# Kernel optimization log

Hardware: AMD Instinct MI355X
Metric: run time of the kernel (lower is better)

Reference implementation:

```python
import jax, jax.numpy as jnp
import numpy as np

N, E = 100000, 250000
SD, CD = 128, 768


def setup_inputs() -> dict:
    key = jax.random.key(0)
    ks = jax.random.split(key, 12)
    z = jax.random.normal(ks[0], (N, SD), dtype=jnp.float32)
    chemistry = jax.random.normal(ks[1], (N, CD), dtype=jnp.float32)
    edge = jax.random.randint(ks[2], (E, 2), 0, N, dtype=jnp.int64)
    smiles_mask = (jax.random.uniform(ks[3], (N,)) < 0.8).astype(jnp.float32)
    s = 1.0 / np.sqrt(SD)
    W1s = jax.random.uniform(ks[4], (SD, SD // 2), jnp.float32, -s, s)
    b1s = jax.random.uniform(ks[5], (SD // 2,), jnp.float32, -s, s)
    s2 = 1.0 / np.sqrt(SD // 2)
    W2s = jax.random.uniform(ks[6], (SD // 2, 1), jnp.float32, -s2, s2)
    b2s = jax.random.uniform(ks[7], (1,), jnp.float32, -s2, s2)
    c = 1.0 / np.sqrt(CD)
    W1c = jax.random.uniform(ks[8], (CD, CD // 4), jnp.float32, -c, c)
    b1c = jax.random.uniform(ks[9], (CD // 4,), jnp.float32, -c, c)
    c2 = 1.0 / np.sqrt(CD // 4)
    W2c = jax.random.uniform(ks[10], (CD // 4, 1), jnp.float32, -c2, c2)
    b2c = jax.random.uniform(ks[11], (1,), jnp.float32, -c2, c2)
    alpha = jnp.float32(0.1)
    return {"z": z, "chemistry": chemistry, "edge": edge, "smiles_mask": smiles_mask,
            "W1s": W1s, "b1s": b1s, "W2s": W2s, "b2s": b2s,
            "W1c": W1c, "b1c": b1c, "W2c": W2c, "b2c": b2c, "alpha": alpha}


def reference(z, chemistry, edge, smiles_mask, W1s, b1s, W2s, b2s,
              W1c, b1c, W2c, b2c, alpha):
    src, dst = edge[:, 0], edge[:, 1]
    # structural branch: gather, product, 2-layer MLP (dropout = eval identity)
    structural_prod = z[src] * z[dst]                      # [E, SD]
    h_s = jax.nn.relu(structural_prod @ W1s + b1s)         # [E, SD//2]
    score_structural = (h_s @ W2s + b2s)[:, 0]             # [E]
    # chemical branch
    chemical_prod = chemistry[src] * chemistry[dst]        # [E, CD]
    h_c = jax.nn.relu(chemical_prod @ W1c + b1c)           # [E, CD//4]
    score_chemical = (h_c @ W2c + b2c)[:, 0]               # [E]
    both_valid = smiles_mask[src] * smiles_mask[dst]       # [E]
    score_chemical = both_valid * score_chemical
    return score_structural + alpha * score_chemical
```

## Files before the change

### kernel.cpp

```cpp
#include <hip/hip_runtime.h>
#include <hip/hip_bf16.h>
#include <stdint.h>

#define N_NODES 100000
#define NE      250000
#define SDIM    128
#define CDIM    768
#define HS      64
#define HC      192
#define TILE_E  32
#define NBLK    ((NE + TILE_E - 1) / TILE_E)

#define CT2     32
#define NT2     ((NE + CT2 - 1) / CT2)
#define CBLK2   256

typedef __attribute__((ext_vector_type(8))) short bf16x8;
typedef __attribute__((ext_vector_type(4))) float f32x4;

static __device__ __forceinline__ uint16_t f2bf(float f) {
    union { __hip_bfloat16 h; uint16_t u; } cv;
    cv.h = __float2bfloat16(f);
    return cv.u;
}
static __device__ __forceinline__ float bf2f(uint16_t u) {
    union { float f; uint32_t i; } cv; cv.i = ((uint32_t)u) << 16; return cv.f;
}

__global__ void k_convert_w(const float* __restrict__ W1c, uint16_t* __restrict__ W1cT) {
    const int tid = blockIdx.x * 256 + threadIdx.x;
    const int stride = gridDim.x * 256;
    for (int i = tid; i < HC * CDIM; i += stride) {
        const int n = i / CDIM, k = i - n * CDIM;
        W1cT[i] = f2bf(W1c[k * HC + n]);
    }
}

__global__ __launch_bounds__(256, 3) void k_structural(
    const float* __restrict__ z, const int* __restrict__ edge,
    const float* __restrict__ W1s, const float* __restrict__ b1s,
    const float* __restrict__ W2s, const float* __restrict__ b2s,
    const float* __restrict__ smask, const float* __restrict__ alphap,
    float* __restrict__ out, float* __restrict__ valid,
    const float* __restrict__ chem, uint16_t* __restrict__ chem_bf, long conv_n)
{
    __shared__ float Wl[SDIM * HS];
    __shared__ float Pl[TILE_E * 132];

    const int t = threadIdx.x;
    const int e0 = blockIdx.x * TILE_E;

    {
        const float4* src = (const float4*)W1s;
        float4* dst = (float4*)Wl;
        for (int m = t; m < SDIM * HS / 4; m += 256) dst[m] = src[m];
    }
    {
        const int el = t >> 3, p = t & 7;
        const int e = e0 + el;
        if (e < NE) {
            const int s = edge[2 * e], d = edge[2 * e + 1];
            const float* rs = z + (long)s * SDIM;
            const float* rd = z + (long)d * SDIM;
            #pragma unroll
            for (int cc = 0; cc < 2; ++cc) {
                const int c = p + cc * 8;
                float4 s0 = *(const float4*)(rs + c * 8);
                float4 s1 = *(const float4*)(rs + c * 8 + 4);
                float4 d0 = *(const float4*)(rd + c * 8);
                float4 d1 = *(const float4*)(rd + c * 8 + 4);
                float4 r0 = {s0.x * d0.x, s0.y * d0.y, s0.z * d0.z, s0.w * d0.w};
                float4 r1 = {s1.x * d1.x, s1.y * d1.y, s1.z * d1.z, s1.w * d1.w};
                *(float4*)(&Pl[el * 132 + c * 8]) = r0;
                *(float4*)(&Pl[el * 132 + c * 8 + 4]) = r1;
            }
        }
    }
    __syncthreads();

    const int el = t >> 3, p = t & 7;
    float h[8] = {0, 0, 0, 0, 0, 0, 0, 0};
    const float4* Wl4 = (const float4*)Wl;
    #pragma unroll 4
    for (int k = 0; k < SDIM; ++k) {
        const float pv = Pl[el * 132 + k];
        float4 w0 = Wl4[k * 16 + p * 2];
        float4 w1 = Wl4[k * 16 + p * 2 + 1];
        h[0] += pv * w0.x; h[1] += pv * w0.y; h[2] += pv * w0.z; h[3] += pv * w0.w;
        h[4] += pv * w1.x; h[5] += pv * w1.y; h[6] += pv * w1.z; h[7] += pv * w1.w;
    }
    float partial = 0.f;
    #pragma unroll
    for (int j = 0; j < 8; ++j) {
        const int c = p * 8 + j;
        partial += fmaxf(h[j] + b1s[c], 0.f) * W2s[c];
    }
    partial += __shfl_xor(partial, 1);
    partial += __shfl_xor(partial, 2);
    partial += __shfl_xor(partial, 4);
    const int e = e0 + el;
    if (p == 0 && e < NE) {
        out[e] = partial + b2s[0];
        const int s = edge[2 * e], d = edge[2 * e + 1];
        valid[e] = alphap[0] * smask[s] * smask[d];
    }

    {
        const long base = ((long)blockIdx.x * 256 + t) * 8;
        const long stride = (long)gridDim.x * 256 * 8;
        for (long i = base; i < conv_n; i += stride) {
            float4 a = *(const float4*)(chem + i);
            float4 b = *(const float4*)(chem + i + 4);
            union { uint16_t u[8]; int4 v; } pk;
            pk.u[0] = f2bf(a.x); pk.u[1] = f2bf(a.y);
            pk.u[2] = f2bf(a.z); pk.u[3] = f2bf(a.w);
            pk.u[4] = f2bf(b.x); pk.u[5] = f2bf(b.y);
            pk.u[6] = f2bf(b.z); pk.u[7] = f2bf(b.w);
            *(int4*)(chem_bf + i) = pk.v;
        }
    }
}

static __device__ __forceinline__ void cvt_store_bf(uint16_t* Abuf, int el, int ch,
                                                    int4 vs, int4 vd) {
    union { int4 v; uint16_t u[8]; } a, b, r;
    a.v = vs; b.v = vd;
    #pragma unroll
    for (int q = 0; q < 8; ++q) r.u[q] = f2bf(bf2f(a.u[q]) * bf2f(b.u[q]));
    const int byte = el * 1536 + ((ch * 16) ^ ((el & 7) << 4));
    *(int4*)((char*)Abuf + byte) = r.v;
}
static __device__ __forceinline__ void zero_store(uint16_t* Abuf, int el, int ch) {
    const int byte = el * 1536 + ((ch * 16) ^ ((el & 7) << 4));
    int4 z = {0, 0, 0, 0};
    *(int4*)((char*)Abuf + byte) = z;
}
static __device__ __forceinline__ void stage_f32(uint16_t* Abuf, int el, int ch,
                                                 const float* rs, const float* rd) {
    float4 a0 = *(const float4*)(rs + ch * 8);
    float4 a1 = *(const float4*)(rs + ch * 8 + 4);
    float4 b0 = *(const float4*)(rd + ch * 8);
    float4 b1 = *(const float4*)(rd + ch * 8 + 4);
    union { int4 v; uint16_t u[8]; } r;
    r.u[0] = f2bf(a0.x * b0.x); r.u[1] = f2bf(a0.y * b0.y);
    r.u[2] = f2bf(a0.z * b0.z); r.u[3] = f2bf(a0.w * b0.w);
    r.u[4] = f2bf(a1.x * b1.x); r.u[5] = f2bf(a1.y * b1.y);
    r.u[6] = f2bf(a1.z * b1.z); r.u[7] = f2bf(a1.w * b1.w);
    const int byte = el * 1536 + ((ch * 16) ^ ((el & 7) << 4));
    *(int4*)((char*)Abuf + byte) = r.v;
}

template<bool BF16TAB>
__global__ __launch_bounds__(768, 3) void k_chem_v6(
    const void* __restrict__ chemv, const int* __restrict__ edge,
    const uint16_t* __restrict__ W1cT, const float* __restrict__ b1c,
    const float* __restrict__ W2c, const float* __restrict__ b2c,
    const float* __restrict__ valid, float* __restrict__ out)
{
    __shared__ uint16_t A[2][CT2 * CDIM];
    __shared__ float xchg[6][64][20];
    __shared__ float part[2][CT2][8];
    __shared__ int   ebuf[2][2 * CT2];

    const int t = threadIdx.x;
    const int w = t >> 6, lane = t & 63, lr = lane & 15, lg = lane >> 4;
    const int cg = w >> 1, kh = w & 1;
    const int b = blockIdx.x;

    const int t0 = b * 30 + (b < 133 ? b : 133);
    const int t1 = t0 + 30 + (b < 133 ? 1 : 0);

    const uint16_t* chemB = (const uint16_t*)chemv;
    const float*    chemF = (const float*)chemv;

    bf16x8 Breg[24];
    #pragma unroll
    for (int ct = 0; ct < 2; ++ct) {
        const uint16_t* Bp = W1cT + (long)(cg * 32 + ct * 16 + lr) * CDIM + kh * 384 + lg * 8;
        #pragma unroll
        for (int kc = 0; kc < 12; ++kc)
            Breg[ct * 12 + kc] = *(const bf16x8*)(Bp + kc * 32);
    }
    #pragma unroll
    for (int i = 0; i < 24; ++i) asm volatile("" : "+v"(Breg[i]));

    float b1v[2], w2v[2];
    #pragma unroll
    for (int ct = 0; ct < 2; ++ct) {
        b1v[ct] = b1c[cg * 32 + ct * 16 + lr];
        w2v[ct] = W2c[cg * 32 + ct * 16 + lr];
    }
    const float b2 = b2c[0];

    const int elb = t / 96;
    const int ch  = t % 96;

    #pragma unroll
    for (int q = 0; q < 4; ++q) {
        const int el = elb + 8 * q;
        const int e  = t0 * CT2 + el;
        const bool ok = (e < NE);
        const int ee = ok ? e : 0;
        const int si = edge[2 * ee], di = edge[2 * ee + 1];
        if constexpr (BF16TAB) {
            int4 vs = *(const int4*)(chemB + (long)si * CDIM + ch * 8);
            int4 vd = *(const int4*)(chemB + (long)di * CDIM + ch * 8);
            if (ok) cvt_store_bf(A[0], el, ch, vs, vd);
            else    zero_store(A[0], el, ch);
        } else {
            if (ok) stage_f32(A[0], el, ch, chemF + (long)si * CDIM, chemF + (long)di * CDIM);
            else    zero_store(A[0], el, ch);
        }
    }
    if (t < CT2) {
        const int e = (t0 + 1) * CT2 + t;
        const int ee = (e < NE) ? e : 0;
        int2 p2 = *(const int2*)(edge + 2 * ee);
        *(int2*)&ebuf[(t0 + 1) & 1][2 * t] = p2;
    }
    float vld_cur = 0.f, vld_next = 0.f;
    if (t < CT2) {
        const int e = t0 * CT2 + t;
        vld_next = (e < NE) ? valid[e] : 0.f;
    }
    __syncthreads();

    const int swz = (lr & 7) << 4;
    const int rb0 = lr * 1536;
    const int rb1 = rb0 + 16 * 1536;

    for (int ti = t0; ti < t1; ++ti) {
        const int it = ti - t0, cur = it & 1;
        const bool pf  = (ti + 1 < t1);
        const bool pf2 = (ti + 2 < t1);

        if (pf) {
            uint16_t* dst = A[cur ^ 1];
            const int ebase = (ti + 1) * CT2;
            const int par = (ti + 1) & 1;
            int2 e0p = *(const int2*)&ebuf[par][2 * elb];
            int2 e1p = *(const int2*)&ebuf[par][2 * (elb + 8)];
            int2 e2p = *(const int2*)&ebuf[par][2 * (elb + 16)];
            int2 e3p = *(const int2*)&ebuf[par][2 * (elb + 24)];
            if constexpr (BF16TAB) {
                {
                    int4 vs0 = *(const int4*)(chemB + (long)e0p.x * CDIM + ch * 8);
                    int4 vd0 = *(const int4*)(chemB + (long)e0p.y * CDIM + ch * 8);
                    int4 vs1 = *(const int4*)(chemB + (long)e1p.x * CDIM + ch * 8);
                    int4 vd1 = *(const int4*)(chemB + (long)e1p.y * CDIM + ch * 8);
                    if (ebase + elb < NE)     cvt_store_bf(dst, elb,     ch, vs0, vd0);
                    else                      zero_store(dst, elb, ch);
                    if (ebase + elb + 8 < NE) cvt_store_bf(dst, elb + 8, ch, vs1, vd1);
                    else                      zero_store(dst, elb + 8, ch);
                }
                {
                    int4 vs2 = *(const int4*)(chemB + (long)e2p.x * CDIM + ch * 8);
                    int4 vd2 = *(const int4*)(chemB + (long)e2p.y * CDIM + ch * 8);
                    int4 vs3 = *(const int4*)(chemB + (long)e3p.x * CDIM + ch * 8);
                    int4 vd3 = *(const int4*)(chemB + (long)e3p.y * CDIM + ch * 8);
                    if (ebase + elb + 16 < NE) cvt_store_bf(dst, elb + 16, ch, vs2, vd2);
                    else                       zero_store(dst, elb + 16, ch);
                    if (ebase + elb + 24 < NE) cvt_store_bf(dst, elb + 24, ch, vs3, vd3);
                    else                       zero_store(dst, elb + 24, ch);
                }
            } else {
                #pragma unroll
                for (int q = 0; q < 4; ++q) {
                    const int el = elb + 8 * q;
                    int2 ep = (q == 0) ? e0p : (q == 1) ? e1p : (q == 2) ? e2p : e3p;
                    if (ebase + el < NE)
                        stage_f32(dst, el, ch, chemF + (long)ep.x * CDIM,
                                  chemF + (long)ep.y * CDIM);
                    else zero_store(dst, el, ch);
                }
            }
        }
        if (pf2 && t < CT2) {
            const int e = (ti + 2) * CT2 + t;
            const int ee = (e < NE) ? e : 0;
            int2 p2 = *(const int2*)(edge + 2 * ee);
            *(int2*)&ebuf[ti & 1][2 * t] = p2;
        }

        if (ti > t0 && t < CT2) {
            const int e = (ti - 1) * CT2 + t;
            if (e < NE) {
                float s_ = 0.f;
                #pragma unroll
                for (int c6 = 0; c6 < 6; ++c6) s_ += part[cur ^ 1][t][c6];
                atomicAdd(&out[e], vld_cur * (s_ + b2));
            }
        }
        if (t < CT2) {
            vld_cur = vld_next;
            if (pf) {
                const int e = (ti + 1) * CT2 + t;
                vld_next = (e < NE) ? valid[e] : 0.f;
            }
        }

        f32x4 acc00 = {0,0,0,0}, acc01 = {0,0,0,0}, acc10 = {0,0,0,0}, acc11 = {0,0,0,0};
        {
            const char* Ab = (const char*)A[cur];
            #pragma unroll
            for (int kc = 0; kc < 12; ++kc) {
                const int off = ((kh * 12 + kc) * 64 + lg * 16) ^ swz;
                bf16x8 a0 = *(const bf16x8*)(Ab + rb0 + off);
                bf16x8 a1 = *(const bf16x8*)(Ab + rb1 + off);
                acc00 = __builtin_amdgcn_mfma_f32_16x16x32_bf16(a0, Breg[kc],      acc00, 0, 0, 0);
                acc10 = __builtin_amdgcn_mfma_f32_16x16x32_bf16(a1, Breg[kc],      acc10, 0, 0, 0);
                acc01 = __builtin_amdgcn_mfma_f32_16x16x32_bf16(a0, Breg[12 + kc], acc01, 0, 0, 0);
                acc11 = __builtin_amdgcn_mfma_f32_16x16x32_bf16(a1, Breg[12 + kc], acc11, 0, 0, 0);
            }
        }

        if (kh == 1) {
            float* xp = xchg[cg][lane];
            *(float4*)(xp +  0) = (float4){acc00[0], acc00[1], acc00[2], acc00[3]};
            *(float4*)(xp +  4) = (float4){acc01[0], acc01[1], acc01[2], acc01[3]};
            *(float4*)(xp +  8) = (float4){acc10[0], acc10[1], acc10[2], acc10[3]};
            *(float4*)(xp + 12) = (float4){acc11[0], acc11[1], acc11[2], acc11[3]};
        }
        __syncthreads();
        if (kh == 0) {
            const float* xp = xchg[cg][lane];
            float4 x0 = *(const float4*)(xp + 0);
            float4 x1 = *(const float4*)(xp + 4);
            float4 x2 = *(const float4*)(xp + 8);
            float4 x3 = *(const float4*)(xp + 12);
            acc00[0] += x0.x; acc00[1] += x0.y; acc00[2] += x0.z; acc00[3] += x0.w;
            acc01[0] += x1.x; acc01[1] += x1.y; acc01[2] += x1.z; acc01[3] += x1.w;
            acc10[0] += x2.x; acc10[1] += x2.y; acc10[2] += x2.z; acc10[3] += x2.w;
            acc11[0] += x3.x; acc11[1] += x3.y; acc11[2] += x3.z; acc11[3] += x3.w;
            #pragma unroll
            for (int r = 0; r < 4; ++r) {
                float p0 = fmaxf(acc00[r] + b1v[0], 0.f) * w2v[0]
                         + fmaxf(acc01[r] + b1v[1], 0.f) * w2v[1];
                float p1 = fmaxf(acc10[r] + b1v[0], 0.f) * w2v[0]
                         + fmaxf(acc11[r] + b1v[1], 0.f) * w2v[1];
                #pragma unroll
                for (int m = 1; m <= 8; m <<= 1) {
                    p0 += __shfl_xor(p0, m);
                    p1 += __shfl_xor(p1, m);
                }
                if (lr == 0) {
                    part[cur][lg * 4 + r][cg]      = p0;
                    part[cur][16 + lg * 4 + r][cg] = p1;
                }
            }
        }
        __syncthreads();
    }

    if (t < CT2) {
        const int e = (t1 - 1) * CT2 + t;
        if (e < NE) {
            const int cur = (t1 - 1 - t0) & 1;
            float s_ = 0.f;
            #pragma unroll
            for (int c6 = 0; c6 < 6; ++c6) s_ += part[cur][t][c6];
            atomicAdd(&out[e], vld_cur * (s_ + b2));
        }
    }
}

extern "C" void kernel_launch(void* const* d_in, const int* in_sizes, int n_in,
                              void* d_out, int out_size, void* d_ws, size_t ws_size,
                              hipStream_t stream)
{
    const float* z     = (const float*)d_in[0];
    const float* chem  = (const float*)d_in[1];
    const int*   edge  = (const int*)d_in[2];
    const float* smask = (const float*)d_in[3];
    const float* W1s   = (const float*)d_in[4];
    const float* b1s   = (const float*)d_in[5];
    const float* W2s   = (const float*)d_in[6];
    const float* b2s   = (const float*)d_in[7];
    const float* W1c   = (const float*)d_in[8];
    const float* b1c   = (const float*)d_in[9];
    const float* W2c   = (const float*)d_in[10];
    const float* b2c   = (const float*)d_in[11];
    const float* alpha = (const float*)d_in[12];
    float* out = (float*)d_out;

    uint16_t* W1cT   = (uint16_t*)d_ws;
    uint16_t* chemBf = (uint16_t*)d_ws + (size_t)HC * CDIM;
    const size_t bfBytes = (size_t)N_NODES * CDIM * 2;
    const size_t needBf  = (size_t)HC * CDIM * 2 + bfBytes + (size_t)NE * 4;
    const bool useBf = ws_size >= needBf;
    float* valid = useBf
        ? (float*)((char*)d_ws + (size_t)HC * CDIM * 2 + bfBytes)
        : (float*)((char*)d_ws + (size_t)HC * CDIM * 2);
    const long conv_n = useBf ? (long)N_NODES * CDIM : 0;

    k_convert_w<<<dim3(64), dim3(256), 0, stream>>>(W1c, W1cT);

    k_structural<<<dim3(NBLK), dim3(256), 0, stream>>>(
        z, edge, W1s, b1s, W2s, b2s, smask, alpha, out, valid, chem, chemBf, conv_n);

    if (useBf)
        k_chem_v6<true><<<dim3(CBLK2), dim3(768), 0, stream>>>(
            (const void*)chemBf, edge, W1cT, b1c, W2c, b2c, valid, out);
    else
        k_chem_v6<false><<<dim3(CBLK2), dim3(768), 0, stream>>>(
            (const void*)chem, edge, W1cT, b1c, W2c, b2c, valid, out);
}
```

Measured before the change: 326.3 us.

## Prefetch chemistry rows via async global-to-LDS loads with 16-edge tiles

```diff
diff --git a/kernel.cpp b/kernel.cpp
--- a/kernel.cpp
+++ b/kernel.cpp
@@ -11,8 +11,11 @@
 #define TILE_E  32
 #define NBLK    ((NE + TILE_E - 1) / TILE_E)
 
+#define CT3     16
+#define NT3     (NE / CT3)
+#define CBLK3   256
+
 #define CT2     32
-#define NT2     ((NE + CT2 - 1) / CT2)
 #define CBLK2   256
 
 typedef __attribute__((ext_vector_type(8))) short bf16x8;
@@ -25,6 +28,11 @@
 }
 static __device__ __forceinline__ float bf2f(uint16_t u) {
     union { float f; uint32_t i; } cv; cv.i = ((uint32_t)u) << 16; return cv.f;
+}
+static __device__ __forceinline__ void gload_lds16(const void* g, void* l) {
+    __builtin_amdgcn_global_load_lds(
+        (const __attribute__((address_space(1))) void*)g,
+        (__attribute__((address_space(3))) void*)l, 16, 0, 0);
 }
 
 __global__ void k_convert_w(const float* __restrict__ W1c, uint16_t* __restrict__ W1cT) {
@@ -36,13 +44,30 @@
     }
 }
 
+__global__ __launch_bounds__(256) void k_convert_chem(
+    const float* __restrict__ chem, uint16_t* __restrict__ chemBf)
+{
+    const long total = (long)N_NODES * CDIM;
+    const long i0 = ((long)blockIdx.x * 256 + threadIdx.x) * 8;
+    const long stride = (long)gridDim.x * 256 * 8;
+    for (long i = i0; i < total; i += stride) {
+        float4 a = *(const float4*)(chem + i);
+        float4 b = *(const float4*)(chem + i + 4);
+        union { uint16_t u[8]; int4 v; } pk;
+        pk.u[0] = f2bf(a.x); pk.u[1] = f2bf(a.y);
+        pk.u[2] = f2bf(a.z); pk.u[3] = f2bf(a.w);
+        pk.u[4] = f2bf(b.x); pk.u[5] = f2bf(b.y);
+        pk.u[6] = f2bf(b.z); pk.u[7] = f2bf(b.w);
+        *(int4*)(chemBf + i) = pk.v;
+    }
+}
+
 __global__ __launch_bounds__(256, 3) void k_structural(
     const float* __restrict__ z, const int* __restrict__ edge,
     const float* __restrict__ W1s, const float* __restrict__ b1s,
     const float* __restrict__ W2s, const float* __restrict__ b2s,
     const float* __restrict__ smask, const float* __restrict__ alphap,
-    float* __restrict__ out, float* __restrict__ valid,
-    const float* __restrict__ chem, uint16_t* __restrict__ chem_bf, long conv_n)
+    float* __restrict__ out, float* __restrict__ valid)
 {
     __shared__ float Wl[SDIM * HS];
     __shared__ float Pl[TILE_E * 132];
@@ -104,21 +129,6 @@
         const int s = edge[2 * e], d = edge[2 * e + 1];
         valid[e] = alphap[0] * smask[s] * smask[d];
     }
-
-    {
-        const long base = ((long)blockIdx.x * 256 + t) * 8;
-        const long stride = (long)gridDim.x * 256 * 8;
-        for (long i = base; i < conv_n; i += stride) {
-            float4 a = *(const float4*)(chem + i);
-            float4 b = *(const float4*)(chem + i + 4);
-            union { uint16_t u[8]; int4 v; } pk;
-            pk.u[0] = f2bf(a.x); pk.u[1] = f2bf(a.y);
-            pk.u[2] = f2bf(a.z); pk.u[3] = f2bf(a.w);
-            pk.u[4] = f2bf(b.x); pk.u[5] = f2bf(b.y);
-            pk.u[6] = f2bf(b.z); pk.u[7] = f2bf(b.w);
-            *(int4*)(chem_bf + i) = pk.v;
-        }
-    }
 }
 
 static __device__ __forceinline__ void cvt_store_bf(uint16_t* Abuf, int el, int ch,
@@ -132,8 +142,8 @@
 }
 static __device__ __forceinline__ void zero_store(uint16_t* Abuf, int el, int ch) {
     const int byte = el * 1536 + ((ch * 16) ^ ((el & 7) << 4));
-    int4 z = {0, 0, 0, 0};
-    *(int4*)((char*)Abuf + byte) = z;
+    int4 zv = {0, 0, 0, 0};
+    *(int4*)((char*)Abuf + byte) = zv;
 }
 static __device__ __forceinline__ void stage_f32(uint16_t* Abuf, int el, int ch,
                                                  const float* rs, const float* rd) {
@@ -150,9 +160,166 @@
     *(int4*)((char*)Abuf + byte) = r.v;
 }
 
-template<bool BF16TAB>
-__global__ __launch_bounds__(768, 3) void k_chem_v6(
-    const void* __restrict__ chemv, const int* __restrict__ edge,
+__global__ __launch_bounds__(768, 3) void k_chem_v8(
+    const uint16_t* __restrict__ chemB, const int* __restrict__ edge,
+    const uint16_t* __restrict__ W1cT, const float* __restrict__ b1c,
+    const float* __restrict__ W2c, const float* __restrict__ b2c,
+    const float* __restrict__ valid, float* __restrict__ out)
+{
+    __shared__ uint16_t A[2][CT3 * CDIM];
+    __shared__ uint16_t raw[CT3 * 2 * CDIM];
+    __shared__ float xchg[6][64][12];
+    __shared__ float part[2][CT3][8];
+    __shared__ int   ebuf[2][2 * CT3];
+
+    const int t = threadIdx.x;
+    const int w = t >> 6, lane = t & 63, lr = lane & 15, lg = lane >> 4;
+    const int cg = w >> 1, kh = w & 1;
+    const int b = blockIdx.x;
+
+    const int t0 = b * 61 + (b < 9 ? b : 9);
+    const int t1 = t0 + 61 + (b < 9 ? 1 : 0);
+
+    bf16x8 Breg[24];
+    #pragma unroll
+    for (int ct = 0; ct < 2; ++ct) {
+        const uint16_t* Bp = W1cT + (long)(cg * 32 + ct * 16 + lr) * CDIM + kh * 384 + lg * 8;
+        #pragma unroll
+        for (int kc = 0; kc < 12; ++kc)
+            Breg[ct * 12 + kc] = *(const bf16x8*)(Bp + kc * 32);
+    }
+    #pragma unroll
+    for (int i = 0; i < 24; ++i) asm volatile("" : "+v"(Breg[i]));
+
+    float b1v[2], w2v[2];
+    #pragma unroll
+    for (int ct = 0; ct < 2; ++ct) {
+        b1v[ct] = b1c[cg * 32 + ct * 16 + lr];
+        w2v[ct] = W2c[cg * 32 + ct * 16 + lr];
+    }
+    const float b2 = b2c[0];
+
+    int rj[4], offj[4];
+    #pragma unroll
+    for (int j = 0; j < 4; ++j) {
+        const int off = (w * 4 + j) * 1024 + lane * 16;
+        rj[j]   = off / 1536;
+        offj[j] = off - rj[j] * 1536;
+    }
+
+    #pragma unroll
+    for (int q = 0; q < 2; ++q) {
+        const int slot = t + q * 768;
+        const int el = slot / 96, ch = slot - (slot / 96) * 96;
+        const int e = t0 * CT3 + el;
+        const int si = edge[2 * e], di = edge[2 * e + 1];
+        int4 vs = *(const int4*)(chemB + (long)si * CDIM + ch * 8);
+        int4 vd = *(const int4*)(chemB + (long)di * CDIM + ch * 8);
+        cvt_store_bf(A[0], el, ch, vs, vd);
+    }
+    if (t < 2 * CT3 && t0 + 1 < t1) {
+        const int e = (t0 + 1) * CT3 + (t >> 1);
+        ebuf[(t0 + 1) & 1][t] = edge[2 * e + (t & 1)];
+    }
+    float vld_cur = 0.f, vld_next = 0.f;
+    if (t < CT3) vld_next = valid[t0 * CT3 + t];
+    __syncthreads();
+
+    const int swz = (lr & 7) << 4;
+    const int rb0 = lr * 1536;
+
+    for (int ti = t0; ti < t1; ++ti) {
+        const int cur = (ti - t0) & 1;
+        const bool pf  = (ti + 1 < t1);
+        const bool pf2 = (ti + 2 < t1);
+
+        if (pf) {
+            const int par = (ti + 1) & 1;
+            #pragma unroll
+            for (int j = 0; j < 4; ++j) {
+                const int node = ebuf[par][rj[j]];
+                const uint16_t* g = chemB + (long)node * CDIM + (offj[j] >> 1);
+                char* l = (char*)raw + (w * 4 + j) * 1024;
+                gload_lds16(g, l);
+            }
+        }
+
+        if (pf2 && t < 2 * CT3) {
+            const int e = (ti + 2) * CT3 + (t >> 1);
+            ebuf[ti & 1][t] = edge[2 * e + (t & 1)];
+        }
+
+        if (ti > t0 && t < CT3) {
+            const int e = (ti - 1) * CT3 + t;
+            float s_ = 0.f;
+            #pragma unroll
+            for (int c6 = 0; c6 < 6; ++c6) s_ += part[cur ^ 1][t][c6];
+            atomicAdd(&out[e], vld_cur * (s_ + b2));
+        }
+        if (t < CT3) {
+            vld_cur = vld_next;
+            if (pf) vld_next = valid[(ti + 1) * CT3 + t];
+        }
+
+        f32x4 acc0 = {0, 0, 0, 0}, acc1 = {0, 0, 0, 0};
+        {
+            const char* Ab = (const char*)A[cur];
+            #pragma unroll
+            for (int kc = 0; kc < 12; ++kc) {
+                const int off = ((kh * 12 + kc) * 64 + lg * 16) ^ swz;
+                bf16x8 a0 = *(const bf16x8*)(Ab + rb0 + off);
+                acc0 = __builtin_amdgcn_mfma_f32_16x16x32_bf16(a0, Breg[kc],      acc0, 0, 0, 0);
+                acc1 = __builtin_amdgcn_mfma_f32_16x16x32_bf16(a0, Breg[12 + kc], acc1, 0, 0, 0);
+            }
+        }
+
+        if (kh == 1) {
+            float* xp = xchg[cg][lane];
+            *(float4*)(xp + 0) = (float4){acc0[0], acc0[1], acc0[2], acc0[3]};
+            *(float4*)(xp + 4) = (float4){acc1[0], acc1[1], acc1[2], acc1[3]};
+        }
+        __syncthreads();
+        if (kh == 0) {
+            const float* xp = xchg[cg][lane];
+            float4 x0 = *(const float4*)(xp + 0);
+            float4 x1 = *(const float4*)(xp + 4);
+            acc0[0] += x0.x; acc0[1] += x0.y; acc0[2] += x0.z; acc0[3] += x0.w;
+            acc1[0] += x1.x; acc1[1] += x1.y; acc1[2] += x1.z; acc1[3] += x1.w;
+            #pragma unroll
+            for (int r = 0; r < 4; ++r) {
+                float p0 = fmaxf(acc0[r] + b1v[0], 0.f) * w2v[0]
+                         + fmaxf(acc1[r] + b1v[1], 0.f) * w2v[1];
+                #pragma unroll
+                for (int m = 1; m <= 8; m <<= 1) p0 += __shfl_xor(p0, m);
+                if (lr == 0) part[cur][lg * 4 + r][cg] = p0;
+            }
+        }
+
+        if (pf) {
+            #pragma unroll
+            for (int q = 0; q < 2; ++q) {
+                const int slot = t + q * 768;
+                const int el = slot / 96, ch = slot - (slot / 96) * 96;
+                int4 vs = *(const int4*)((const char*)raw + (el * 2 + 0) * 1536 + ch * 16);
+                int4 vd = *(const int4*)((const char*)raw + (el * 2 + 1) * 1536 + ch * 16);
+                cvt_store_bf(A[cur ^ 1], el, ch, vs, vd);
+            }
+        }
+        __syncthreads();
+    }
+
+    if (t < CT3) {
+        const int e = (t1 - 1) * CT3 + t;
+        const int cur = (t1 - 1 - t0) & 1;
+        float s_ = 0.f;
+        #pragma unroll
+        for (int c6 = 0; c6 < 6; ++c6) s_ += part[cur][t][c6];
+        atomicAdd(&out[e], vld_cur * (s_ + b2));
+    }
+}
+
+__global__ __launch_bounds__(768, 3) void k_chem_fb(
+    const float* __restrict__ chemF, const int* __restrict__ edge,
     const uint16_t* __restrict__ W1cT, const float* __restrict__ b1c,
     const float* __restrict__ W2c, const float* __restrict__ b2c,
     const float* __restrict__ valid, float* __restrict__ out)
@@ -170,9 +337,6 @@
     const int t0 = b * 30 + (b < 133 ? b : 133);
     const int t1 = t0 + 30 + (b < 133 ? 1 : 0);
 
-    const uint16_t* chemB = (const uint16_t*)chemv;
-    const float*    chemF = (const float*)chemv;
-
     bf16x8 Breg[24];
     #pragma unroll
     for (int ct = 0; ct < 2; ++ct) {
@@ -202,15 +366,8 @@
         const bool ok = (e < NE);
         const int ee = ok ? e : 0;
         const int si = edge[2 * ee], di = edge[2 * ee + 1];
-        if constexpr (BF16TAB) {
-            int4 vs = *(const int4*)(chemB + (long)si * CDIM + ch * 8);
-            int4 vd = *(const int4*)(chemB + (long)di * CDIM + ch * 8);
-            if (ok) cvt_store_bf(A[0], el, ch, vs, vd);
-            else    zero_store(A[0], el, ch);
-        } else {
-            if (ok) stage_f32(A[0], el, ch, chemF + (long)si * CDIM, chemF + (long)di * CDIM);
-            else    zero_store(A[0], el, ch);
-        }
+        if (ok) stage_f32(A[0], el, ch, chemF + (long)si * CDIM, chemF + (long)di * CDIM);
+        else    zero_store(A[0], el, ch);
     }
     if (t < CT2) {
         const int e = (t0 + 1) * CT2 + t;
@@ -230,7 +387,7 @@
     const int rb1 = rb0 + 16 * 1536;
 
     for (int ti = t0; ti < t1; ++ti) {
-        const int it = ti - t0, cur = it & 1;
+        const int cur = (ti - t0) & 1;
         const bool pf  = (ti + 1 < t1);
         const bool pf2 = (ti + 2 < t1);
 
@@ -238,41 +395,13 @@
             uint16_t* dst = A[cur ^ 1];
             const int ebase = (ti + 1) * CT2;
             const int par = (ti + 1) & 1;
-            int2 e0p = *(const int2*)&ebuf[par][2 * elb];
-            int2 e1p = *(const int2*)&ebuf[par][2 * (elb + 8)];
-            int2 e2p = *(const int2*)&ebuf[par][2 * (elb + 16)];
-            int2 e3p = *(const int2*)&ebuf[par][2 * (elb + 24)];
-            if constexpr (BF16TAB) {
-                {
-                    int4 vs0 = *(const int4*)(chemB + (long)e0p.x * CDIM + ch * 8);
-                    int4 vd0 = *(const int4*)(chemB + (long)e0p.y * CDIM + ch * 8);
-                    int4 vs1 = *(const int4*)(chemB + (long)e1p.x * CDIM + ch * 8);
-                    int4 vd1 = *(const int4*)(chemB + (long)e1p.y * CDIM + ch * 8);
-                    if (ebase + elb < NE)     cvt_store_bf(dst, elb,     ch, vs0, vd0);
-                    else                      zero_store(dst, elb, ch);
-                    if (ebase + elb + 8 < NE) cvt_store_bf(dst, elb + 8, ch, vs1, vd1);
-                    else                      zero_store(dst, elb + 8, ch);
-                }
-                {
-                    int4 vs2 = *(const int4*)(chemB + (long)e2p.x * CDIM + ch * 8);
-                    int4 vd2 = *(const int4*)(chemB + (long)e2p.y * CDIM + ch * 8);
-                    int4 vs3 = *(const int4*)(chemB + (long)e3p.x * CDIM + ch * 8);
-                    int4 vd3 = *(const int4*)(chemB + (long)e3p.y * CDIM + ch * 8);
-                    if (ebase + elb + 16 < NE) cvt_store_bf(dst, elb + 16, ch, vs2, vd2);
-                    else                       zero_store(dst, elb + 16, ch);
-                    if (ebase + elb + 24 < NE) cvt_store_bf(dst, elb + 24, ch, vs3, vd3);
-                    else                       zero_store(dst, elb + 24, ch);
-                }
-            } else {
-                #pragma unroll
-                for (int q = 0; q < 4; ++q) {
-                    const int el = elb + 8 * q;
-                    int2 ep = (q == 0) ? e0p : (q == 1) ? e1p : (q == 2) ? e2p : e3p;
-                    if (ebase + el < NE)
-                        stage_f32(dst, el, ch, chemF + (long)ep.x * CDIM,
-                                  chemF + (long)ep.y * CDIM);
-                    else zero_store(dst, el, ch);
-                }
+            #pragma unroll
+            for (int q = 0; q < 4; ++q) {
+                const int el = elb + 8 * q;
+                int2 ep = *(const int2*)&ebuf[par][2 * el];
+                if (ebase + el < NE)
+                    stage_f32(dst, el, ch, chemF + (long)ep.x * CDIM, chemF + (long)ep.y * CDIM);
+                else zero_store(dst, el, ch);
             }
         }
         if (pf2 && t < CT2) {
@@ -281,7 +410,6 @@
             int2 p2 = *(const int2*)(edge + 2 * ee);
             *(int2*)&ebuf[ti & 1][2 * t] = p2;
         }
-
         if (ti > t0 && t < CT2) {
             const int e = (ti - 1) * CT2 + t;
             if (e < NE) {
@@ -391,17 +519,19 @@
     float* valid = useBf
         ? (float*)((char*)d_ws + (size_t)HC * CDIM * 2 + bfBytes)
         : (float*)((char*)d_ws + (size_t)HC * CDIM * 2);
-    const long conv_n = useBf ? (long)N_NODES * CDIM : 0;
 
     k_convert_w<<<dim3(64), dim3(256), 0, stream>>>(W1c, W1cT);
 
+    if (useBf)
+        k_convert_chem<<<dim3(2048), dim3(256), 0, stream>>>(chem, chemBf);
+
     k_structural<<<dim3(NBLK), dim3(256), 0, stream>>>(
-        z, edge, W1s, b1s, W2s, b2s, smask, alpha, out, valid, chem, chemBf, conv_n);
+        z, edge, W1s, b1s, W2s, b2s, smask, alpha, out, valid);
 
     if (useBf)
-        k_chem_v6<true><<<dim3(CBLK2), dim3(768), 0, stream>>>(
-            (const void*)chemBf, edge, W1cT, b1c, W2c, b2c, valid, out);
+        k_chem_v8<<<dim3(CBLK3), dim3(768), 0, stream>>>(
+            chemBf, edge, W1cT, b1c, W2c, b2c, valid, out);
     else
-        k_chem_v6<false><<<dim3(CBLK2), dim3(768), 0, stream>>>(
-            (const void*)chem, edge, W1cT, b1c, W2c, b2c, valid, out);
-}
+        k_chem_fb<<<dim3(CBLK2), dim3(768), 0, stream>>>(
+            chem, edge, W1cT, b1c, W2c, b2c, valid, out);
+}
```

After: 367.9 us. 12.7% more time.
